# Optimization experiments

Hardware: AMD Instinct MI355X
Metric: run time of the kernel (lower is better)

Reference implementation:

```python
import jax, jax.numpy as jnp
import numpy as np

NHEADS = 8
EPS = 1e-6


def setup_inputs() -> dict:
    key = jax.random.key(0)
    ks = jax.random.split(key, 6)
    B, N, H, W = 4, 80, 24, 24
    hidden, guid = 128, 128
    n = B * H * W
    S = 77
    return {
        "query": jax.random.normal(ks[0], (B, N, H, W, hidden + guid), jnp.float32),
        "x": jax.random.normal(ks[1], (n, S, hidden), jnp.float32),
        "guidance": jax.random.normal(ks[2], (n, S, guid), jnp.float32),
        "Wq": jax.random.normal(ks[3], (hidden + guid, hidden), jnp.float32) * (1.0 / np.sqrt(hidden + guid)),
        "bq": jnp.zeros((hidden,), jnp.float32),
        "Wk": jax.random.normal(ks[4], (hidden + guid, hidden), jnp.float32) * (1.0 / np.sqrt(hidden + guid)),
        "bk": jnp.zeros((hidden,), jnp.float32),
        "Wv": jax.random.normal(ks[5], (hidden, hidden), jnp.float32) * (1.0 / np.sqrt(hidden)),
        "bv": jnp.zeros((hidden,), jnp.float32),
    }


def _feature_map(x):
    return jax.nn.elu(x) + 1.0


def reference(query, x, guidance, Wq, bq, Wk, bk, Wv, bv):
    B, N, H, W, C = query.shape
    Dh = Wq.shape[1] // NHEADS  # head dim
    # 'B N H W C -> (B H W) N C'
    qin = query.transpose(0, 2, 3, 1, 4).reshape(B * H * W, N, C)
    q = qin @ Wq + bq                                   # (n, N, hidden)
    k = jnp.concatenate([x, guidance], axis=-1) @ Wk + bk  # (n, S, hidden)
    v = x @ Wv + bv                                     # (n, S, hidden)
    n, S = v.shape[0], v.shape[1]
    q = q.reshape(n, N, NHEADS, Dh)
    k = k.reshape(n, S, NHEADS, Dh)
    v = v.reshape(n, S, NHEADS, Dh)
    Q = _feature_map(q)
    K = _feature_map(k)
    v_scaled = v / S
    KV = jnp.einsum('nshd,nshv->nhdv', K, v_scaled)     # (n, h, d, d)
    Z = 1.0 / (jnp.einsum('nlhd,nhd->nlh', Q, K.sum(axis=1)) + EPS)
    queried = jnp.einsum('nlhd,nhdv,nlh->nlhv', Q, KV, Z) * S  # (n, N, h, d)
    out = queried.mean(axis=1).reshape(n, NHEADS * Dh)  # (n, hidden)
    return out.reshape(B, H, W, NHEADS * Dh)
```

## Files before the change

### kernel.cpp

```cpp
#include <hip/hip_runtime.h>
#include <hip/hip_bf16.h>

typedef __attribute__((ext_vector_type(8))) short bf16x8;
typedef __attribute__((ext_vector_type(4))) float f32x4;

#define S77  77
#define NQ   80
#define KSTR 104
#define XSTR 264
#define QSTR 132

__device__ __forceinline__ unsigned int cvt_pk(float a, float b) {
    union { __hip_bfloat162 h; unsigned int u; } c;
    c.h = __float22bfloat162_rn(make_float2(a, b));
    return c.u;
}
__device__ __forceinline__ unsigned short f2bf(float f) {
    union { __hip_bfloat16 h; unsigned short u; } c;
    c.h = __float2bfloat16(f);
    return c.u;
}

__global__ void transpose_weights(const float* __restrict__ Wq,
                                  const float* __restrict__ Wk,
                                  const float* __restrict__ Wv,
                                  unsigned short* __restrict__ ws) {
    int t = blockIdx.x * 256 + threadIdx.x;
    if (t < 32768) {
        int k = t >> 7, c = t & 127;
        ws[c * 256 + k] = f2bf(Wq[t]);
    } else if (t < 65536) {
        int u = t - 32768; int k = u >> 7, c = u & 127;
        ws[32768 + c * 256 + k] = f2bf(Wk[u]);
    } else if (t < 81920) {
        int u = t - 65536; int k = u >> 7, c = u & 127;
        ws[65536 + c * 128 + k] = f2bf(Wv[u]);
    }
}

__global__ __launch_bounds__(1024, 4)
void attn_kernel(const float* __restrict__ query,
                 const float* __restrict__ x,
                 const float* __restrict__ guid,
                 const unsigned short* __restrict__ wT,
                 const float* __restrict__ bq,
                 const float* __restrict__ bk,
                 const float* __restrict__ bv,
                 float* __restrict__ out)
{
    const int n    = blockIdx.x;
    const int tid  = threadIdx.x;
    const int wid  = tid >> 6;
    const int lane = tid & 63;
    const int quad = lane >> 4;
    const int mr   = lane & 15;

    const int b  = n / 576;
    const int hw = n % 576;

    __shared__ union { unsigned short XGb[NQ * XSTR]; float Qf[NQ * QSTR]; } R0;
    __shared__ union { unsigned short Qb16[NQ * XSTR]; float KV[8][16][16]; } R1;
    __shared__ unsigned short KfT[128 * KSTR];
    __shared__ unsigned short VsT[128 * KSTR];
    __shared__ float Ksum[128];
    __shared__ float Zl[NQ * 8];
    __shared__ float Qb[128];

    const unsigned short* WqT = wT;
    const unsigned short* WkT = wT + 32768;
    const unsigned short* WvT = wT + 65536;
    const f32x4 cZ = {0.f, 0.f, 0.f, 0.f};

    const float* xg = x    + (size_t)n * S77 * 128;
    const float* gg = guid + (size_t)n * S77 * 128;

    if (wid < 8) {
        const float* src = (lane < 32) ? xg : gg;
        const int c4  = (lane & 31) * 4;
        const int col = (lane < 32) ? c4 : (128 + c4);
        float4 buf[10];
        #pragma unroll
        for (int k = 0; k < 10; ++k) {
            const int s = wid + 8 * k;
            if (s < S77) buf[k] = *(const float4*)(src + s * 128 + c4);
        }
        #pragma unroll
        for (int k = 0; k < 10; ++k) {
            const int s = wid + 8 * k;
            if (s < S77) {
                uint2 v; v.x = cvt_pk(buf[k].x, buf[k].y); v.y = cvt_pk(buf[k].z, buf[k].w);
                *(uint2*)&R0.XGb[s * XSTR + col] = v;
            }
        }
    } else {
        const int w8 = wid - 8;
        float4 buf[10];
        #pragma unroll
        for (int k = 0; k < 10; ++k) {
            const int l = w8 + 8 * k;
            buf[k] = *(const float4*)(query + ((size_t)(b * 80 + l) * 576 + hw) * 256 + lane * 4);
        }
        #pragma unroll
        for (int k = 0; k < 10; ++k) {
            const int l = w8 + 8 * k;
            uint2 v; v.x = cvt_pk(buf[k].x, buf[k].y); v.y = cvt_pk(buf[k].z, buf[k].w);
            *(uint2*)&R1.Qb16[l * XSTR + lane * 4] = v;
        }
    }
    __syncthreads();

    f32x4 accD[5];

    if (wid < 8) {
        bf16x8 bfk[8];
        #pragma unroll
        for (int kk = 0; kk < 8; ++kk)
            bfk[kk] = *(const bf16x8*)(WkT + (wid * 16 + mr) * 256 + kk * 32 + quad * 8);
        f32x4 acc[5];
        #pragma unroll
        for (int m = 0; m < 5; ++m) acc[m] = cZ;
        #pragma unroll
        for (int kk = 0; kk < 8; ++kk)
            #pragma unroll
            for (int m = 0; m < 5; ++m) {
                bf16x8 a = *(const bf16x8*)&R0.XGb[(m * 16 + mr) * XSTR + kk * 32 + quad * 8];
                acc[m] = __builtin_amdgcn_mfma_f32_16x16x32_bf16(a, bfk[kk], acc[m], 0, 0, 0);
            }
        const float biask = bk[wid * 16 + mr];
        float ks = 0.f;
        #pragma unroll
        for (int m = 0; m < 5; ++m) {
            float v[4];
            #pragma unroll
            for (int r = 0; r < 4; ++r) {
                const int srow = m * 16 + quad * 4 + r;
                float t = 0.f;
                if (srow < S77) {
                    t = acc[m][r] + biask;
                    t = (t > 0.f) ? (t + 1.f) : __expf(t);
                }
                v[r] = t; ks += t;
            }
            uint2 pv; pv.x = cvt_pk(v[0], v[1]); pv.y = cvt_pk(v[2], v[3]);
            *(uint2*)&KfT[(wid * 16 + mr) * KSTR + m * 16 + quad * 4] = pv;
        }
        ks += __shfl_down(ks, 32); ks += __shfl_down(ks, 16);
        if (lane < 16) Ksum[wid * 16 + mr] = ks;

        bf16x8 bfv[4];
        #pragma unroll
        for (int kk = 0; kk < 4; ++kk)
            bfv[kk] = *(const bf16x8*)(WvT + (wid * 16 + mr) * 128 + kk * 32 + quad * 8);
        #pragma unroll
        for (int m = 0; m < 5; ++m) acc[m] = cZ;
        #pragma unroll
        for (int kk = 0; kk < 4; ++kk)
            #pragma unroll
            for (int m = 0; m < 5; ++m) {
                bf16x8 a = *(const bf16x8*)&R0.XGb[(m * 16 + mr) * XSTR + kk * 32 + quad * 8];
                acc[m] = __builtin_amdgcn_mfma_f32_16x16x32_bf16(a, bfv[kk], acc[m], 0, 0, 0);
            }
        const float biasv = bv[wid * 16 + mr];
        #pragma unroll
        for (int m = 0; m < 5; ++m) {
            float v[4];
            #pragma unroll
            for (int r = 0; r < 4; ++r) {
                const int srow = m * 16 + quad * 4 + r;
                v[r] = (srow < S77) ? (acc[m][r] + biasv) : 0.f;
            }
            uint2 pv; pv.x = cvt_pk(v[0], v[1]); pv.y = cvt_pk(v[2], v[3]);
            *(uint2*)&VsT[(wid * 16 + mr) * KSTR + m * 16 + quad * 4] = pv;
        }
        {
            const int c = tid >> 2, part = tid & 3;
            const uint2 z = {0u, 0u};
            *(uint2*)&KfT[c * KSTR + 80 + part * 4] = z;
            *(uint2*)&VsT[c * KSTR + 80 + part * 4] = z;
        }
    } else {
        const int w2 = wid - 8;
        bf16x8 bfq[8];
        #pragma unroll
        for (int kk = 0; kk < 8; ++kk)
            bfq[kk] = *(const bf16x8*)(WqT + (w2 * 16 + mr) * 256 + kk * 32 + quad * 8);
        #pragma unroll
        for (int m = 0; m < 5; ++m) accD[m] = cZ;
        #pragma unroll
        for (int kk = 0; kk < 8; ++kk)
            #pragma unroll
            for (int m = 0; m < 5; ++m) {
                bf16x8 a = *(const bf16x8*)&R1.Qb16[(m * 16 + mr) * XSTR + kk * 32 + quad * 8];
                accD[m] = __builtin_amdgcn_mfma_f32_16x16x32_bf16(a, bfq[kk], accD[m], 0, 0, 0);
            }
    }
    __syncthreads();

    if (wid < 8) {
        const int h = wid;
        f32x4 acc = cZ;
        #pragma unroll
        for (int ks3 = 0; ks3 < 3; ++ks3) {
            const int sc = ks3 * 32 + quad * 8;
            bf16x8 a  = *(const bf16x8*)&KfT[(h * 16 + mr) * KSTR + sc];
            bf16x8 bb = *(const bf16x8*)&VsT[(h * 16 + mr) * KSTR + sc];
            acc = __builtin_amdgcn_mfma_f32_16x16x32_bf16(a, bb, acc, 0, 0, 0);
        }
        #pragma unroll
        for (int r = 0; r < 4; ++r) R1.KV[h][quad * 4 + r][mr] = acc[r];
    } else {
        const int w2 = wid - 8;
        const float biasq = bq[w2 * 16 + mr];
        #pragma unroll
        for (int m = 0; m < 5; ++m)
            #pragma unroll
            for (int r = 0; r < 4; ++r) {
                const int lrow = m * 16 + quad * 4 + r;
                float v = accD[m][r] + biasq;
                v = (v > 0.f) ? (v + 1.f) : __expf(v);
                R0.Qf[lrow * QSTR + w2 * 16 + mr] = v;
            }
    }
    __syncthreads();

    if (tid < NQ * 8) {
        const int l = tid >> 3, h = tid & 7;
        float d = 0.f;
        #pragma unroll
        for (int j = 0; j < 16; ++j) d += R0.Qf[l * QSTR + h * 16 + j] * Ksum[h * 16 + j];
        Zl[tid] = 1.f / (d + 1e-6f);
    }
    __syncthreads();

    {
        const int p = tid >> 3;
        const int g = tid & 7;
        const int h = p >> 4;
        float s = 0.f;
        #pragma unroll
        for (int l = g * 10; l < g * 10 + 10; ++l)
            s += Zl[l * 8 + h] * R0.Qf[l * QSTR + p];
        s += __shfl_xor(s, 4); s += __shfl_xor(s, 2); s += __shfl_xor(s, 1);
        if (g == 0) Qb[p] = s;
    }
    __syncthreads();

    if (tid < 128) {
        const int h = tid >> 4, e = tid & 15;
        float o = 0.f;
        #pragma unroll
        for (int d2 = 0; d2 < 16; ++d2) o += Qb[h * 16 + d2] * R1.KV[h][d2][e];
        out[(size_t)n * 128 + tid] = o * (1.f / 80.f);
    }
}

extern "C" void kernel_launch(void* const* d_in, const int* in_sizes, int n_in,
                              void* d_out, int out_size, void* d_ws, size_t ws_size,
                              hipStream_t stream) {
    const float* query = (const float*)d_in[0];
    const float* x     = (const float*)d_in[1];
    const float* g     = (const float*)d_in[2];
    const float* Wq    = (const float*)d_in[3];
    const float* bq    = (const float*)d_in[4];
    const float* Wk    = (const float*)d_in[5];
    const float* bk    = (const float*)d_in[6];
    const float* Wv    = (const float*)d_in[7];
    const float* bv    = (const float*)d_in[8];
    float* out = (float*)d_out;
    unsigned short* ws = (unsigned short*)d_ws;

    hipLaunchKernelGGL(transpose_weights, dim3(320), dim3(256), 0, stream, Wq, Wk, Wv, ws);
    hipLaunchKernelGGL(attn_kernel, dim3(2304), dim3(1024), 0, stream,
                       query, x, g, ws, bq, bk, bv, out);
}
```

Before: 479.2 us.

## Restructure attention kernel to 512 threads with chunked double-buffered staging

Halves the block size to 512 threads and splits the K-dimension of the projections into two 128-wide chunks. Each chunk is staged in bf16 through a small double-buffered shared region, so the next chunk's global loads overlap the current chunk's MFMAs. Shared memory usage drops substantially, which is meant to allow more resident blocks per CU and hide memory latency. Waves now tile rows and columns of the K, V and Q projections, and the Z normalization and the mean over queries are folded into register shuffles instead of extra shared-memory passes. In exchange there are more barriers, serialized K/V then Q phases, and weight fragments reloaded from global inside the inner loops.

```diff
diff --git a/kernel.cpp b/kernel.cpp
--- a/kernel.cpp
+++ b/kernel.cpp
@@ -6,9 +6,10 @@
 
 #define S77  77
 #define NQ   80
-#define KSTR 104
-#define XSTR 264
-#define QSTR 132
+#define CS   136
+#define KS2  104
+
+#define MFMA(a,b,c) __builtin_amdgcn_mfma_f32_16x16x32_bf16((a),(b),(c),0,0,0)
 
 __device__ __forceinline__ unsigned int cvt_pk(float a, float b) {
     union { __hip_bfloat162 h; unsigned int u; } c;
@@ -38,7 +39,7 @@
     }
 }
 
-__global__ __launch_bounds__(1024, 4)
+__global__ __launch_bounds__(512, 4)
 void attn_kernel(const float* __restrict__ query,
                  const float* __restrict__ x,
                  const float* __restrict__ guid,
@@ -54,17 +55,18 @@
     const int lane = tid & 63;
     const int quad = lane >> 4;
     const int mr   = lane & 15;
-
-    const int b  = n / 576;
-    const int hw = n % 576;
-
-    __shared__ union { unsigned short XGb[NQ * XSTR]; float Qf[NQ * QSTR]; } R0;
-    __shared__ union { unsigned short Qb16[NQ * XSTR]; float KV[8][16][16]; } R1;
-    __shared__ unsigned short KfT[128 * KSTR];
-    __shared__ unsigned short VsT[128 * KSTR];
-    __shared__ float Ksum[128];
-    __shared__ float Zl[NQ * 8];
-    __shared__ float Qb[128];
+    const int rg   = wid >> 2;
+    const int cg   = wid & 3;
+    const int b    = n / 576;
+    const int hw   = n % 576;
+    const int r0   = rg * 48;
+
+    __shared__ union {
+        unsigned short stage[2][96 * CS];
+        unsigned short tr[2][128 * KS2];
+        float qbar[256];
+    } U;
+    __shared__ float KsumP[256];
 
     const unsigned short* WqT = wT;
     const unsigned short* WkT = wT + 32768;
@@ -74,183 +76,216 @@
     const float* xg = x    + (size_t)n * S77 * 128;
     const float* gg = guid + (size_t)n * S77 * 128;
 
-    if (wid < 8) {
-        const float* src = (lane < 32) ? xg : gg;
-        const int c4  = (lane & 31) * 4;
-        const int col = (lane < 32) ? c4 : (128 + c4);
-        float4 buf[10];
-        #pragma unroll
-        for (int k = 0; k < 10; ++k) {
-            const int s = wid + 8 * k;
-            if (s < S77) buf[k] = *(const float4*)(src + s * 128 + c4);
-        }
-        #pragma unroll
-        for (int k = 0; k < 10; ++k) {
-            const int s = wid + 8 * k;
-            if (s < S77) {
-                uint2 v; v.x = cvt_pk(buf[k].x, buf[k].y); v.y = cvt_pk(buf[k].z, buf[k].w);
-                *(uint2*)&R0.XGb[s * XSTR + col] = v;
-            }
-        }
-    } else {
-        const int w8 = wid - 8;
-        float4 buf[10];
-        #pragma unroll
-        for (int k = 0; k < 10; ++k) {
-            const int l = w8 + 8 * k;
-            buf[k] = *(const float4*)(query + ((size_t)(b * 80 + l) * 576 + hw) * 256 + lane * 4);
-        }
-        #pragma unroll
-        for (int k = 0; k < 10; ++k) {
-            const int l = w8 + 8 * k;
-            uint2 v; v.x = cvt_pk(buf[k].x, buf[k].y); v.y = cvt_pk(buf[k].z, buf[k].w);
-            *(uint2*)&R1.Qb16[l * XSTR + lane * 4] = v;
-        }
-    }
-    __syncthreads();
-
-    f32x4 accD[5];
-
-    if (wid < 8) {
-        bf16x8 bfk[8];
-        #pragma unroll
-        for (int kk = 0; kk < 8; ++kk)
-            bfk[kk] = *(const bf16x8*)(WkT + (wid * 16 + mr) * 256 + kk * 32 + quad * 8);
-        f32x4 acc[5];
-        #pragma unroll
-        for (int m = 0; m < 5; ++m) acc[m] = cZ;
-        #pragma unroll
-        for (int kk = 0; kk < 8; ++kk)
-            #pragma unroll
-            for (int m = 0; m < 5; ++m) {
-                bf16x8 a = *(const bf16x8*)&R0.XGb[(m * 16 + mr) * XSTR + kk * 32 + quad * 8];
-                acc[m] = __builtin_amdgcn_mfma_f32_16x16x32_bf16(a, bfk[kk], acc[m], 0, 0, 0);
-            }
-        const float biask = bk[wid * 16 + mr];
-        float ks = 0.f;
-        #pragma unroll
-        for (int m = 0; m < 5; ++m) {
-            float v[4];
+    const int srow = tid >> 5;
+    const int seg  = tid & 31;
+
+    float4 sb[5];
+
+    f32x4 Kacc[3][2], Vacc[3][2];
+    #pragma unroll
+    for (int i = 0; i < 3; ++i) {
+        Kacc[i][0] = cZ; Kacc[i][1] = cZ;
+        Vacc[i][0] = cZ; Vacc[i][1] = cZ;
+    }
+
+    #pragma unroll
+    for (int it = 0; it < 5; ++it) {
+        const int s = srow + it * 16;
+        if (s < S77) sb[it] = *(const float4*)(xg + (size_t)s * 128 + seg * 4);
+    }
+    #pragma unroll
+    for (int it = 0; it < 5; ++it) {
+        const int s = srow + it * 16;
+        if (s < S77) {
+            uint2 p; p.x = cvt_pk(sb[it].x, sb[it].y); p.y = cvt_pk(sb[it].z, sb[it].w);
+            *(uint2*)&U.stage[0][s * CS + seg * 4] = p;
+        }
+    }
+    __syncthreads();
+
+    #pragma unroll
+    for (int c = 0; c < 2; ++c) {
+        if (c == 0) {
+            #pragma unroll
+            for (int it = 0; it < 5; ++it) {
+                const int s = srow + it * 16;
+                if (s < S77) sb[it] = *(const float4*)(gg + (size_t)s * 128 + seg * 4);
+            }
+        }
+        const unsigned short* sbase = U.stage[c];
+        #pragma unroll
+        for (int kk = 0; kk < 4; ++kk) {
+            const int kloc  = kk * 32 + quad * 8;
+            const int kglob = c * 128 + kk * 32;
+            bf16x8 a0 = *(const bf16x8*)&sbase[(r0      + mr) * CS + kloc];
+            bf16x8 a1 = *(const bf16x8*)&sbase[(r0 + 16 + mr) * CS + kloc];
+            bf16x8 a2;
+            if (rg == 0) a2 = *(const bf16x8*)&sbase[(32 + mr) * CS + kloc];
+            #pragma unroll
+            for (int t = 0; t < 2; ++t) {
+                const int cc = cg * 32 + t * 16 + mr;
+                bf16x8 bkf = *(const bf16x8*)(WkT + cc * 256 + kglob + quad * 8);
+                Kacc[0][t] = MFMA(a0, bkf, Kacc[0][t]);
+                Kacc[1][t] = MFMA(a1, bkf, Kacc[1][t]);
+                if (rg == 0) Kacc[2][t] = MFMA(a2, bkf, Kacc[2][t]);
+                if (c == 0) {
+                    bf16x8 bvf = *(const bf16x8*)(WvT + cc * 128 + kglob + quad * 8);
+                    Vacc[0][t] = MFMA(a0, bvf, Vacc[0][t]);
+                    Vacc[1][t] = MFMA(a1, bvf, Vacc[1][t]);
+                    if (rg == 0) Vacc[2][t] = MFMA(a2, bvf, Vacc[2][t]);
+                }
+            }
+        }
+        if (c == 0) {
+            #pragma unroll
+            for (int it = 0; it < 5; ++it) {
+                const int s = srow + it * 16;
+                if (s < S77) {
+                    uint2 p; p.x = cvt_pk(sb[it].x, sb[it].y); p.y = cvt_pk(sb[it].z, sb[it].w);
+                    *(uint2*)&U.stage[1][s * CS + seg * 4] = p;
+                }
+            }
+        }
+        __syncthreads();
+    }
+
+    #pragma unroll
+    for (int t = 0; t < 2; ++t) {
+        const int cc = cg * 32 + t * 16 + mr;
+        const float biask = bk[cc];
+        const float biasv = bv[cc];
+        float ksp = 0.f;
+        #pragma unroll
+        for (int mt = 0; mt < 3; ++mt) {
+            const int s0 = r0 + mt * 16 + quad * 4;
+            float kv4[4], vv4[4];
             #pragma unroll
             for (int r = 0; r < 4; ++r) {
-                const int srow = m * 16 + quad * 4 + r;
-                float t = 0.f;
-                if (srow < S77) {
-                    t = acc[m][r] + biask;
-                    t = (t > 0.f) ? (t + 1.f) : __expf(t);
+                const int s = s0 + r;
+                float tk = 0.f, tv = 0.f;
+                if (s < S77) {
+                    tk = Kacc[mt][t][r] + biask;
+                    tk = (tk > 0.f) ? (tk + 1.f) : __expf(tk);
+                    tv = Vacc[mt][t][r] + biasv;
                 }
-                v[r] = t; ks += t;
-            }
-            uint2 pv; pv.x = cvt_pk(v[0], v[1]); pv.y = cvt_pk(v[2], v[3]);
-            *(uint2*)&KfT[(wid * 16 + mr) * KSTR + m * 16 + quad * 4] = pv;
-        }
-        ks += __shfl_down(ks, 32); ks += __shfl_down(ks, 16);
-        if (lane < 16) Ksum[wid * 16 + mr] = ks;
-
-        bf16x8 bfv[4];
-        #pragma unroll
-        for (int kk = 0; kk < 4; ++kk)
-            bfv[kk] = *(const bf16x8*)(WvT + (wid * 16 + mr) * 128 + kk * 32 + quad * 8);
-        #pragma unroll
-        for (int m = 0; m < 5; ++m) acc[m] = cZ;
-        #pragma unroll
-        for (int kk = 0; kk < 4; ++kk)
-            #pragma unroll
-            for (int m = 0; m < 5; ++m) {
-                bf16x8 a = *(const bf16x8*)&R0.XGb[(m * 16 + mr) * XSTR + kk * 32 + quad * 8];
-                acc[m] = __builtin_amdgcn_mfma_f32_16x16x32_bf16(a, bfv[kk], acc[m], 0, 0, 0);
-            }
-        const float biasv = bv[wid * 16 + mr];
-        #pragma unroll
-        for (int m = 0; m < 5; ++m) {
-            float v[4];
-            #pragma unroll
-            for (int r = 0; r < 4; ++r) {
-                const int srow = m * 16 + quad * 4 + r;
-                v[r] = (srow < S77) ? (acc[m][r] + biasv) : 0.f;
-            }
-            uint2 pv; pv.x = cvt_pk(v[0], v[1]); pv.y = cvt_pk(v[2], v[3]);
-            *(uint2*)&VsT[(wid * 16 + mr) * KSTR + m * 16 + quad * 4] = pv;
-        }
-        {
-            const int c = tid >> 2, part = tid & 3;
-            const uint2 z = {0u, 0u};
-            *(uint2*)&KfT[c * KSTR + 80 + part * 4] = z;
-            *(uint2*)&VsT[c * KSTR + 80 + part * 4] = z;
-        }
-    } else {
-        const int w2 = wid - 8;
-        bf16x8 bfq[8];
-        #pragma unroll
-        for (int kk = 0; kk < 8; ++kk)
-            bfq[kk] = *(const bf16x8*)(WqT + (w2 * 16 + mr) * 256 + kk * 32 + quad * 8);
-        #pragma unroll
-        for (int m = 0; m < 5; ++m) accD[m] = cZ;
-        #pragma unroll
-        for (int kk = 0; kk < 8; ++kk)
-            #pragma unroll
-            for (int m = 0; m < 5; ++m) {
-                bf16x8 a = *(const bf16x8*)&R1.Qb16[(m * 16 + mr) * XSTR + kk * 32 + quad * 8];
-                accD[m] = __builtin_amdgcn_mfma_f32_16x16x32_bf16(a, bfq[kk], accD[m], 0, 0, 0);
-            }
-    }
-    __syncthreads();
-
-    if (wid < 8) {
-        const int h = wid;
-        f32x4 acc = cZ;
-        #pragma unroll
-        for (int ks3 = 0; ks3 < 3; ++ks3) {
-            const int sc = ks3 * 32 + quad * 8;
-            bf16x8 a  = *(const bf16x8*)&KfT[(h * 16 + mr) * KSTR + sc];
-            bf16x8 bb = *(const bf16x8*)&VsT[(h * 16 + mr) * KSTR + sc];
-            acc = __builtin_amdgcn_mfma_f32_16x16x32_bf16(a, bb, acc, 0, 0, 0);
-        }
-        #pragma unroll
-        for (int r = 0; r < 4; ++r) R1.KV[h][quad * 4 + r][mr] = acc[r];
-    } else {
-        const int w2 = wid - 8;
-        const float biasq = bq[w2 * 16 + mr];
-        #pragma unroll
-        for (int m = 0; m < 5; ++m)
-            #pragma unroll
-            for (int r = 0; r < 4; ++r) {
-                const int lrow = m * 16 + quad * 4 + r;
-                float v = accD[m][r] + biasq;
-                v = (v > 0.f) ? (v + 1.f) : __expf(v);
-                R0.Qf[lrow * QSTR + w2 * 16 + mr] = v;
-            }
-    }
-    __syncthreads();
-
-    if (tid < NQ * 8) {
-        const int l = tid >> 3, h = tid & 7;
-        float d = 0.f;
-        #pragma unroll
-        for (int j = 0; j < 16; ++j) d += R0.Qf[l * QSTR + h * 16 + j] * Ksum[h * 16 + j];
-        Zl[tid] = 1.f / (d + 1e-6f);
+                kv4[r] = tk; vv4[r] = tv; ksp += tk;
+            }
+            uint2 pk_; pk_.x = cvt_pk(kv4[0], kv4[1]); pk_.y = cvt_pk(kv4[2], kv4[3]);
+            *(uint2*)&U.tr[0][cc * KS2 + s0] = pk_;
+            uint2 pv_; pv_.x = cvt_pk(vv4[0], vv4[1]); pv_.y = cvt_pk(vv4[2], vv4[3]);
+            *(uint2*)&U.tr[1][cc * KS2 + s0] = pv_;
+        }
+        ksp += __shfl_xor(ksp, 16);
+        ksp += __shfl_xor(ksp, 32);
+        if (quad == 0) KsumP[rg * 128 + cc] = ksp;
+    }
+
+    #pragma unroll
+    for (int it = 0; it < 5; ++it) {
+        const int l = srow + it * 16;
+        sb[it] = *(const float4*)(query + ((size_t)(b * 80 + l) * 576 + hw) * 256 + seg * 4);
+    }
+    __syncthreads();
+
+    f32x4 KVacc = cZ;
+    #pragma unroll
+    for (int ks3 = 0; ks3 < 3; ++ks3) {
+        const int sc = ks3 * 32 + quad * 8;
+        bf16x8 a  = *(const bf16x8*)&U.tr[0][(wid * 16 + mr) * KS2 + sc];
+        bf16x8 bb = *(const bf16x8*)&U.tr[1][(wid * 16 + mr) * KS2 + sc];
+        KVacc = MFMA(a, bb, KVacc);
+    }
+    __syncthreads();
+
+    f32x4 Qacc[3][2];
+    #pragma unroll
+    for (int i = 0; i < 3; ++i) { Qacc[i][0] = cZ; Qacc[i][1] = cZ; }
+
+    #pragma unroll
+    for (int it = 0; it < 5; ++it) {
+        const int l = srow + it * 16;
+        uint2 p; p.x = cvt_pk(sb[it].x, sb[it].y); p.y = cvt_pk(sb[it].z, sb[it].w);
+        *(uint2*)&U.stage[0][l * CS + seg * 4] = p;
+    }
+    __syncthreads();
+
+    #pragma unroll
+    for (int c = 0; c < 2; ++c) {
+        if (c == 0) {
+            #pragma unroll
+            for (int it = 0; it < 5; ++it) {
+                const int l = srow + it * 16;
+                sb[it] = *(const float4*)(query + ((size_t)(b * 80 + l) * 576 + hw) * 256 + 128 + seg * 4);
+            }
+        }
+        const unsigned short* sbase = U.stage[c];
+        #pragma unroll
+        for (int kk = 0; kk < 4; ++kk) {
+            const int kloc  = kk * 32 + quad * 8;
+            const int kglob = c * 128 + kk * 32;
+            bf16x8 a0 = *(const bf16x8*)&sbase[(r0      + mr) * CS + kloc];
+            bf16x8 a1 = *(const bf16x8*)&sbase[(r0 + 16 + mr) * CS + kloc];
+            bf16x8 a2;
+            if (rg == 0) a2 = *(const bf16x8*)&sbase[(32 + mr) * CS + kloc];
+            #pragma unroll
+            for (int t = 0; t < 2; ++t) {
+                const int cc = cg * 32 + t * 16 + mr;
+                bf16x8 bqf = *(const bf16x8*)(WqT + cc * 256 + kglob + quad * 8);
+                Qacc[0][t] = MFMA(a0, bqf, Qacc[0][t]);
+                Qacc[1][t] = MFMA(a1, bqf, Qacc[1][t]);
+                if (rg == 0) Qacc[2][t] = MFMA(a2, bqf, Qacc[2][t]);
+            }
+        }
+        if (c == 0) {
+            #pragma unroll
+            for (int it = 0; it < 5; ++it) {
+                const int l = srow + it * 16;
+                uint2 p; p.x = cvt_pk(sb[it].x, sb[it].y); p.y = cvt_pk(sb[it].z, sb[it].w);
+                *(uint2*)&U.stage[1][l * CS + seg * 4] = p;
+            }
+        }
+        __syncthreads();
+    }
+
+    #pragma unroll
+    for (int t = 0; t < 2; ++t) {
+        const int cc = cg * 32 + t * 16 + mr;
+        const float biasq = bq[cc];
+        const float ksc = KsumP[cc] + KsumP[128 + cc];
+        float qb = 0.f;
+        #pragma unroll
+        for (int mt = 0; mt < 3; ++mt) {
+            if (!(rg == 1 && mt == 2)) {
+                #pragma unroll
+                for (int r = 0; r < 4; ++r) {
+                    float qv = Qacc[mt][t][r] + biasq;
+                    qv = (qv > 0.f) ? (qv + 1.f) : __expf(qv);
+                    float den = qv * ksc;
+                    den += __shfl_xor(den, 1);
+                    den += __shfl_xor(den, 2);
+                    den += __shfl_xor(den, 4);
+                    den += __shfl_xor(den, 8);
+                    qb += qv * (1.f / (den + 1e-6f));
+                }
+            }
+        }
+        qb += __shfl_xor(qb, 16);
+        qb += __shfl_xor(qb, 32);
+        if (quad == 0) U.qbar[rg * 128 + cc] = qb;
     }
     __syncthreads();
 
     {
-        const int p = tid >> 3;
-        const int g = tid & 7;
-        const int h = p >> 4;
-        float s = 0.f;
-        #pragma unroll
-        for (int l = g * 10; l < g * 10 + 10; ++l)
-            s += Zl[l * 8 + h] * R0.Qf[l * QSTR + p];
-        s += __shfl_xor(s, 4); s += __shfl_xor(s, 2); s += __shfl_xor(s, 1);
-        if (g == 0) Qb[p] = s;
-    }
-    __syncthreads();
-
-    if (tid < 128) {
-        const int h = tid >> 4, e = tid & 15;
         float o = 0.f;
         #pragma unroll
-        for (int d2 = 0; d2 < 16; ++d2) o += Qb[h * 16 + d2] * R1.KV[h][d2][e];
-        out[(size_t)n * 128 + tid] = o * (1.f / 80.f);
+        for (int r = 0; r < 4; ++r) {
+            const int d = wid * 16 + quad * 4 + r;
+            const float qbar = U.qbar[d] + U.qbar[128 + d];
+            o += qbar * KVacc[r];
+        }
+        o += __shfl_xor(o, 16);
+        o += __shfl_xor(o, 32);
+        if (quad == 0) out[(size_t)n * 128 + wid * 16 + mr] = o * (1.f / 80.f);
     }
 }
 
@@ -270,6 +305,6 @@
     unsigned short* ws = (unsigned short*)d_ws;
 
     hipLaunchKernelGGL(transpose_weights, dim3(320), dim3(256), 0, stream, Wq, Wk, Wv, ws);
-    hipLaunchKernelGGL(attn_kernel, dim3(2304), dim3(1024), 0, stream,
+    hipLaunchKernelGGL(attn_kernel, dim3(2304), dim3(512), 0, stream,
                        query, x, g, ws, bq, bk, bv, out);
 }
```

Result: faster. 465.9 us (-2.8%).
